# Performance work log

Measured on AMD Instinct MI355X. Metric: run time of the kernel, lower is better.

Reference implementation:

```python
import jax, jax.numpy as jnp
import numpy as np

N_NODES = 100000


def _sage_conv(x, src, dst, W_l, b, W_r):
    """PyG SAGEConv with mean aggregation: lin_l(mean_{j in N(i)} x_j) + lin_r(x_i).
    edge_index[0]=src (message source j), edge_index[1]=dst (target i)."""
    n = x.shape[0]
    # sum of neighbor features per target node, then divide by in-degree
    agg = jax.ops.segment_sum(x[src], dst, num_segments=n)  # [N, F]
    deg = jax.ops.segment_sum(jnp.ones_like(dst, dtype=x.dtype), dst, num_segments=n)
    agg = agg / jnp.maximum(deg, 1.0)[:, None]
    return agg @ W_l + b + x @ W_r


def setup_inputs() -> dict:
    key = jax.random.key(0)
    ks = jax.random.split(key, 8)
    in_c, hid, out = 128, 128, 2
    sc = lambda f: 1.0 / np.sqrt(f)
    x = jax.random.normal(ks[0], (N_NODES, in_c), dtype=jnp.float32)
    edge_index = jax.random.randint(ks[1], (2, 1600000), 0, N_NODES, dtype=jnp.int64)
    return {
        "x": x,
        "edge_index": edge_index,
        "W1_l": jax.random.normal(ks[2], (in_c, hid), dtype=jnp.float32) * sc(in_c),
        "b1": jnp.zeros((hid,), dtype=jnp.float32),
        "W1_r": jax.random.normal(ks[3], (in_c, hid), dtype=jnp.float32) * sc(in_c),
        "W2_l": jax.random.normal(ks[4], (hid, hid), dtype=jnp.float32) * sc(hid),
        "b2": jnp.zeros((hid,), dtype=jnp.float32),
        "W2_r": jax.random.normal(ks[5], (hid, hid), dtype=jnp.float32) * sc(hid),
        "W_fc": jax.random.normal(ks[6], (hid, out), dtype=jnp.float32) * sc(hid),
        "b_fc": jnp.zeros((out,), dtype=jnp.float32),
    }


def reference(x, edge_index, W1_l, b1, W1_r, W2_l, b2, W2_r, W_fc, b_fc):
    src, dst = edge_index[0], edge_index[1]
    # eval mode: dropout is identity
    h = jax.nn.relu(_sage_conv(x, src, dst, W1_l, b1, W1_r))
    h = jax.nn.relu(_sage_conv(h, src, dst, W2_l, b2, W2_r))
    return h @ W_fc + b_fc
```

## Files before the change

### kernel.cpp

```cpp
#include <hip/hip_runtime.h>

#define NF 128
#define SH 9
#define BNODES 512
#define MAXNB 256

typedef unsigned short u16;
typedef unsigned int u32;
using u16x4 = __attribute__((ext_vector_type(4))) u16;
using u16x8 = __attribute__((ext_vector_type(8))) u16;
using s16x8 = __attribute__((ext_vector_type(8))) short;
using f32x4 = __attribute__((ext_vector_type(4))) float;
using u32x4 = __attribute__((ext_vector_type(4))) u32;
using i32x4 = __attribute__((ext_vector_type(4))) int;

__device__ inline float b2f(u16 b) {
    union { u32 u; float f; } c; c.u = (u32)b << 16; return c.f;
}
__device__ inline float lo2f(u32 w) {
    union { u32 u; float f; } c; c.u = w << 16; return c.f;
}
__device__ inline float hi2f(u32 w) {
    union { u32 u; float f; } c; c.u = w & 0xFFFF0000u; return c.f;
}
__device__ inline u16 f2b(float f) {
    union { float f; u32 u; } c; c.f = f;
    u32 u = c.u;
    u += 0x7FFFu + ((u >> 16) & 1u);
    return (u16)(u >> 16);
}
__device__ inline u16x8 nt_load8(const u16* p) {
    u32x4 v = __builtin_nontemporal_load((const u32x4*)p);
    return *(u16x8*)&v;
}
__device__ inline void nt_store8(u16* p, u16x8 v) {
    __builtin_nontemporal_store(*(u32x4*)&v, (u32x4*)p);
}
__device__ inline int padded4(int d) { return (d + 3) & ~3; }

__global__ __launch_bounds__(256) void bhist_kernel(const int* __restrict__ dst,
                                                    int* __restrict__ bcnt, int E, int NB) {
    __shared__ int h[MAXNB];
    int t = threadIdx.x;
    h[t] = 0;
    __syncthreads();
    for (int e = blockIdx.x * 256 + t; e < E; e += gridDim.x * 256)
        atomicAdd(&h[__builtin_nontemporal_load(dst + e) >> SH], 1);
    __syncthreads();
    if (t < NB && h[t]) atomicAdd(&bcnt[t], h[t]);
}

__global__ __launch_bounds__(256) void bscan_kernel(const int* __restrict__ bcnt,
                                                    int* __restrict__ boff,
                                                    int* __restrict__ gcur, int NB, int E) {
    __shared__ int ss[256];
    int t = threadIdx.x;
    int v = (t < NB) ? bcnt[t] : 0;
    ss[t] = v; __syncthreads();
    for (int off = 1; off < 256; off <<= 1) {
        int u = (t >= off) ? ss[t - off] : 0;
        __syncthreads();
        ss[t] += u;
        __syncthreads();
    }
    int excl = ss[t] - v;
    if (t < NB) { boff[t] = excl; gcur[t] = excl; }
    if (t == 0) boff[NB] = E;
}

__global__ __launch_bounds__(256) void scan_excl_kernel(int* __restrict__ a, int nb) {
    __shared__ int ss[256];
    int t = threadIdx.x;
    int v = (t < nb) ? a[t] : 0;
    ss[t] = v; __syncthreads();
    for (int off = 1; off < 256; off <<= 1) {
        int u = (t >= off) ? ss[t - off] : 0;
        __syncthreads();
        ss[t] += u;
        __syncthreads();
    }
    if (t < nb) a[t] = ss[t] - v;
}

__global__ __launch_bounds__(256) void scatter_kernel(
    const int* __restrict__ src, const int* __restrict__ dst,
    int* __restrict__ gcur, u32* __restrict__ pairs, int E, int NB)
{
    __shared__ int hist[MAXNB];
    __shared__ int cstart[256];
    __shared__ int gbase[MAXNB];
    __shared__ u32 stage[4096];
    __shared__ u16 bmap[4096];
    int t = threadIdx.x;
    int base = blockIdx.x * 4096;

    hist[t] = 0;
    __syncthreads();

    u32 packed[16]; int bb[16]; int loff[16];
    #pragma unroll
    for (int j = 0; j < 16; j++) {
        int e = base + j * 256 + t;
        bb[j] = -1;
        if (e < E) {
            int d = __builtin_nontemporal_load(dst + e);
            int s = __builtin_nontemporal_load(src + e);
            int b = d >> SH;
            bb[j] = b;
            packed[j] = ((u32)(d & (BNODES - 1)) << 17) | (u32)s;
            loff[j] = atomicAdd(&hist[b], 1);
        }
    }
    __syncthreads();

    int hv = hist[t];
    cstart[t] = hv; __syncthreads();
    for (int off = 1; off < 256; off <<= 1) {
        int u = (t >= off) ? cstart[t - off] : 0;
        __syncthreads();
        cstart[t] += u;
        __syncthreads();
    }
    int excl = cstart[t] - hv;
    if (t < NB && hv > 0) gbase[t] = atomicAdd(&gcur[t], hv);
    __syncthreads();
    cstart[t] = excl;
    __syncthreads();

    #pragma unroll
    for (int j = 0; j < 16; j++) if (bb[j] >= 0) {
        int pos = cstart[bb[j]] + loff[j];
        stage[pos] = packed[j];
        bmap[pos] = (u16)bb[j];
    }
    __syncthreads();

    int total = min(4096, E - base);
    for (int k = t; k < total; k += 256) {
        u32 p = stage[k];
        int b = bmap[k];
        pairs[gbase[b] + (k - cstart[b])] = p;
    }
}

__global__ __launch_bounds__(256) void degb_kernel(const u32* __restrict__ pairs,
                                                   const int* __restrict__ boff,
                                                   int* __restrict__ deg,
                                                   int* __restrict__ bsumB, int n) {
    __shared__ int dl[BNODES];
    __shared__ int red[256];
    int b = blockIdx.x, t = threadIdx.x;
    for (int i = t; i < BNODES; i += 256) dl[i] = 0;
    __syncthreads();
    int s = boff[b], e = boff[b + 1];
    for (int k = s + t; k < e; k += 256)
        atomicAdd(&dl[__builtin_nontemporal_load(pairs + k) >> 17], 1);
    __syncthreads();
    int nb0 = b << SH;
    int ps = 0;
    for (int i = t; i < BNODES; i += 256) {
        int d = dl[i];
        if (nb0 + i < n) { deg[nb0 + i] = d; ps += padded4(d); }
    }
    red[t] = ps; __syncthreads();
    for (int off = 128; off; off >>= 1) {
        if (t < off) red[t] += red[t + off];
        __syncthreads();
    }
    if (!t) bsumB[b] = red[0];
}

__global__ __launch_bounds__(256) void fillC_kernel(const u32* __restrict__ pairs,
                                                    const int* __restrict__ boff,
                                                    const int* __restrict__ deg,
                                                    const int* __restrict__ bbase,
                                                    int* __restrict__ info,
                                                    int* __restrict__ adj, int n) {
    __shared__ int begl[BNODES];
    __shared__ int curl[BNODES];
    __shared__ int ss[256];
    int b = blockIdx.x, t = threadIdx.x;
    int nb0 = b << SH;
    int i0 = 2 * t, i1 = 2 * t + 1;
    int d0 = 0, d1 = 0;
    if (nb0 + i0 < n) d0 = deg[nb0 + i0];
    if (nb0 + i1 < n) d1 = deg[nb0 + i1];
    int p0 = padded4(d0), p1 = padded4(d1);
    int s = p0 + p1;
    ss[t] = s; __syncthreads();
    for (int off = 1; off < 256; off <<= 1) {
        int u = (t >= off) ? ss[t - off] : 0;
        __syncthreads();
        ss[t] += u;
        __syncthreads();
    }
    int beg0 = bbase[b] + ss[t] - s;
    int beg1 = beg0 + p0;
    if (nb0 + i1 < n) {
        i32x4 w = {beg0, d0, beg1, d1};
        ((i32x4*)info)[(nb0 >> 1) + t] = w;
    } else if (nb0 + i0 < n) {
        info[2 * (nb0 + i0)] = beg0; info[2 * (nb0 + i0) + 1] = d0;
    }
    begl[i0] = beg0; curl[i0] = 0;
    begl[i1] = beg1; curl[i1] = 0;
    if (nb0 + i0 < n) for (int p = d0; p < p0; p++) adj[beg0 + p] = n;
    if (nb0 + i1 < n) for (int p = d1; p < p1; p++) adj[beg1 + p] = n;
    __syncthreads();
    int sE = boff[b], eE = boff[b + 1];
    for (int k = sE + t; k < eE; k += 256) {
        u32 p = __builtin_nontemporal_load(pairs + k);
        int ld = p >> 17, sr = p & 0x1FFFF;
        int pos = atomicAdd(&curl[ld], 1);
        adj[begl[ld] + pos] = sr;
    }
}

__global__ __launch_bounds__(256) void cast_x_kernel(const float* __restrict__ x,
                                                     u16* __restrict__ xb, int n, int nr) {
    int i = blockIdx.x * 256 + threadIdx.x;
    if (i >= nr * (NF / 8)) return;
    int node = i >> 4, ch = i & 15;
    u16x8 o = (u16x8)0;
    if (node < n) {
        const float* p = x + (size_t)node * NF + ch * 8;
        f32x4 v0 = __builtin_nontemporal_load((const f32x4*)p);
        f32x4 v1 = __builtin_nontemporal_load((const f32x4*)(p + 4));
        o[0] = f2b(v0[0]); o[1] = f2b(v0[1]); o[2] = f2b(v0[2]); o[3] = f2b(v0[3]);
        o[4] = f2b(v1[0]); o[5] = f2b(v1[1]); o[6] = f2b(v1[2]); o[7] = f2b(v1[3]);
    }
    *(u16x8*)(xb + (size_t)node * NF + ch * 8) = o;
}

__global__ void cast_wt_kernel(const float* __restrict__ w0, const float* __restrict__ w1,
                               const float* __restrict__ w2, const float* __restrict__ w3,
                               u16* __restrict__ o0, u16* __restrict__ o1,
                               u16* __restrict__ o2, u16* __restrict__ o3) {
    int m = blockIdx.y;
    const float* w = (m == 0) ? w0 : (m == 1) ? w1 : (m == 2) ? w2 : w3;
    u16* o = (m == 0) ? o0 : (m == 1) ? o1 : (m == 2) ? o2 : o3;
    int i = blockIdx.x * 256 + threadIdx.x;
    int k = i >> 7, nc = i & 127;
    o[nc * NF + k] = f2b(w[k * NF + nc]);
}

template <bool FC>
__global__ __launch_bounds__(512) void sage_fused_kernel(
    const u16* __restrict__ xin,
    const int* __restrict__ info,
    const int* __restrict__ adj,
    const u16* __restrict__ Wtl,
    const u16* __restrict__ Wtr,
    const float* __restrict__ bias,
    const float* __restrict__ Wfc,
    const float* __restrict__ bfc,
    u16* __restrict__ hout,
    float* __restrict__ out,
    int n)
{
    constexpr int MT = 128;
    constexpr int LDK = 136;
    __shared__ u16 A_s[MT][LDK];
    __shared__ u16 W_s[NF][LDK];

    int t = threadIdx.x;
    int node0 = blockIdx.x * MT;

    #pragma unroll
    for (int i = 0; i < 4; i++) {
        int idx = t + i * 512;
        int row = idx >> 4, ch = idx & 15;
        *(u16x8*)&W_s[row][ch * 8] = ((const u16x8*)Wtl)[row * 16 + ch];
    }

    {
        int grp = t >> 4, lane = t & 15;
        const char* xbase = (const char*)xin;
        u32 lo16 = (u32)lane * 16;

        for (int j = 0; j < 4; j++) {
            int m = grp * 4 + j;
            int node = node0 + m;
            float L[4] = {0.f, 0.f, 0.f, 0.f}, H[4] = {0.f, 0.f, 0.f, 0.f};
            int dg = 0;
            if (node < n) {
                int2 inf = *(const int2*)(info + 2 * node);
                dg = inf.y;
                const i32x4* ap = (const i32x4*)(adj + inf.x);
                int ng = (dg + 3) >> 2;

#define ROWU(nb) (*(const u32x4*)(xbase + (((u32)(nb) << 8) + lo16)))
#define ACC4(cur) { \
    u32x4 r0 = ROWU(cur[0]), r1 = ROWU(cur[1]), r2 = ROWU(cur[2]), r3 = ROWU(cur[3]); \
    _Pragma("unroll") \
    for (int k = 0; k < 4; k++) { \
        L[k] += (lo2f(r0[k]) + lo2f(r1[k])) + (lo2f(r2[k]) + lo2f(r3[k])); \
        H[k] += (hi2f(r0[k]) + hi2f(r1[k])) + (hi2f(r2[k]) + hi2f(r3[k])); \
    } }
                i32x4 ia, ib;
                if (ng >= 2) {
                    ia = __builtin_nontemporal_load(ap);
                    ib = __builtin_nontemporal_load(ap + 1);
                }
                int g = 0;
                while (g + 2 <= ng) {
                    i32x4 ca = ia, cb = ib;
                    g += 2;
                    if (g + 2 <= ng) {
                        ia = __builtin_nontemporal_load(ap + g);
                        ib = __builtin_nontemporal_load(ap + g + 1);
                    }
                    ACC4(ca);
                    ACC4(cb);
                }
                if (g < ng) {
                    i32x4 ca = __builtin_nontemporal_load(ap + g);
                    ACC4(ca);
                }
#undef ACC4
#undef ROWU
            }
            float invd = 1.0f / fmaxf((float)dg, 1.0f);
            u16x8 o;
            #pragma unroll
            for (int k = 0; k < 4; k++) {
                o[2 * k]     = f2b(L[k] * invd);
                o[2 * k + 1] = f2b(H[k] * invd);
            }
            *(u16x8*)&A_s[m][lane * 8] = o;
        }
    }
    __syncthreads();

    int l = t & 63;
    int lr = l & 15;
    int lko = (l >> 4) * 8;
    int m0 = (t >> 6) * 16;

    f32x4 acc[8];
    #pragma unroll
    for (int f = 0; f < 8; f++) acc[f] = (f32x4)0.f;

    #pragma unroll
    for (int ks = 0; ks < NF; ks += 32) {
        s16x8 a = *(const s16x8*)&A_s[m0 + lr][ks + lko];
        #pragma unroll
        for (int f = 0; f < 8; f++) {
            s16x8 b = *(const s16x8*)&W_s[f * 16 + lr][ks + lko];
            acc[f] = __builtin_amdgcn_mfma_f32_16x16x32_bf16(a, b, acc[f], 0, 0, 0);
        }
    }
    __syncthreads();

    #pragma unroll
    for (int i = 0; i < 4; i++) {
        int idx = t + i * 512;
        int row = idx >> 4, ch = idx & 15;
        *(u16x8*)&W_s[row][ch * 8] = ((const u16x8*)Wtr)[row * 16 + ch];
    }
    #pragma unroll
    for (int i = 0; i < 4; i++) {
        int idx = t + i * 512;
        int row = idx >> 4, ch = idx & 15;
        int node = node0 + row;
        u16x8 v = (u16x8)0;
        if (node < n) v = nt_load8(xin + (size_t)node * NF + ch * 8);
        *(u16x8*)&A_s[row][ch * 8] = v;
    }
    __syncthreads();

    #pragma unroll
    for (int ks = 0; ks < NF; ks += 32) {
        s16x8 a = *(const s16x8*)&A_s[m0 + lr][ks + lko];
        #pragma unroll
        for (int f = 0; f < 8; f++) {
            s16x8 b = *(const s16x8*)&W_s[f * 16 + lr][ks + lko];
            acc[f] = __builtin_amdgcn_mfma_f32_16x16x32_bf16(a, b, acc[f], 0, 0, 0);
        }
    }

    __syncthreads();
    int rowb = m0 + (l >> 4) * 4;
    #pragma unroll
    for (int f = 0; f < 8; f++) {
        float bc = bias[f * 16 + lr];
        #pragma unroll
        for (int r = 0; r < 4; r++) {
            float v = fmaxf(acc[f][r] + bc, 0.f);
            A_s[rowb + r][f * 16 + lr] = f2b(v);
        }
    }
    __syncthreads();

    if (!FC) {
        #pragma unroll
        for (int i = 0; i < 4; i++) {
            int idx = t + i * 512;
            int row = idx >> 4, ch = idx & 15;
            int node = node0 + row;
            if (node < n)
                nt_store8(hout + (size_t)node * NF + ch * 8, *(u16x8*)&A_s[row][ch * 8]);
            else if (node == n)
                nt_store8(hout + (size_t)node * NF + ch * 8, (u16x8)0);
        }
    } else {
        int g = t >> 5, lane = t & 31;
        float2 wfc[4];
        #pragma unroll
        for (int j = 0; j < 4; j++) wfc[j] = ((const float2*)Wfc)[lane * 4 + j];
        float bf0 = bfc[0], bf1 = bfc[1];
        for (int m8 = 0; m8 < 8; m8++) {
            int m = g * 8 + m8;
            float p0 = 0.f, p1 = 0.f;
            #pragma unroll
            for (int j = 0; j < 4; j++) {
                float h = b2f(A_s[m][lane * 4 + j]);
                p0 += h * wfc[j].x;
                p1 += h * wfc[j].y;
            }
            #pragma unroll
            for (int s = 16; s; s >>= 1) {
                p0 += __shfl_down(p0, s, 32);
                p1 += __shfl_down(p1, s, 32);
            }
            int node = node0 + m;
            if (lane == 0 && node < n)
                *(float2*)(out + (size_t)node * 2) = make_float2(p0 + bf0, p1 + bf1);
        }
    }
}

extern "C" void kernel_launch(void* const* d_in, const int* in_sizes, int n_in,
                              void* d_out, int out_size, void* d_ws, size_t ws_size,
                              hipStream_t stream) {
    const float* x   = (const float*)d_in[0];
    const int*   ei  = (const int*)d_in[1];
    const float* W1l = (const float*)d_in[2];
    const float* b1  = (const float*)d_in[3];
    const float* W1r = (const float*)d_in[4];
    const float* W2l = (const float*)d_in[5];
    const float* b2  = (const float*)d_in[6];
    const float* W2r = (const float*)d_in[7];
    const float* Wfc = (const float*)d_in[8];
    const float* bfc = (const float*)d_in[9];

    const int n = in_sizes[0] / NF;
    const int E = in_sizes[1] / 2;
    const int nr = n + 1;
    const int NB = (n + BNODES - 1) >> SH;
    const int* src = ei;
    const int* dst = ei + E;

    u16* xb     = (u16*)d_ws;
    u16* h1     = xb + (size_t)nr * NF;
    u16* Wt1l   = h1 + (size_t)nr * NF;
    u16* Wt1r   = Wt1l + NF * NF;
    u16* Wt2l   = Wt1r + NF * NF;
    u16* Wt2r   = Wt2l + NF * NF;
    int* adj    = (int*)(Wt2r + NF * NF);
    int* deg    = adj + ((size_t)E + 3 * (size_t)n);
    int* info   = deg + n;
    int* bsumB  = info + 2 * (size_t)n;
    int* bcnt   = bsumB + 256;
    int* gcur   = bcnt + 256;
    int* boff   = gcur + 256;
    u32* pairs  = (u32*)(boff + 257);

    (void)hipMemsetAsync(bcnt, 0, 256 * sizeof(int), stream);

    bhist_kernel<<<1024, 256, 0, stream>>>(dst, bcnt, E, NB);
    bscan_kernel<<<1, 256, 0, stream>>>(bcnt, boff, gcur, NB, E);
    scatter_kernel<<<(E + 4095) / 4096, 256, 0, stream>>>(src, dst, gcur, pairs, E, NB);
    degb_kernel<<<NB, 256, 0, stream>>>(pairs, boff, deg, bsumB, n);
    scan_excl_kernel<<<1, 256, 0, stream>>>(bsumB, NB);
    fillC_kernel<<<NB, 256, 0, stream>>>(pairs, boff, deg, bsumB, info, adj, n);

    cast_x_kernel<<<(nr * (NF / 8) + 255) / 256, 256, 0, stream>>>(x, xb, n, nr);
    cast_wt_kernel<<<dim3(64, 4), 256, 0, stream>>>(W1l, W1r, W2l, W2r,
                                                    Wt1l, Wt1r, Wt2l, Wt2r);

    int fb = (nr + 127) / 128;
    sage_fused_kernel<false><<<fb, 512, 0, stream>>>(
        xb, info, adj, Wt1l, Wt1r, b1, nullptr, nullptr, h1, nullptr, n);
    sage_fused_kernel<true><<<fb, 512, 0, stream>>>(
        h1, info, adj, Wt2l, Wt2r, b2, Wfc, bfc, nullptr, (float*)d_out, n);
}
```

Before: 258.2 us.

## Split fused SAGE layer into separate gather kernel and MFMA GEMM kernel

Result: slower. 263.7 us (+2.1%).

```diff
diff --git a/kernel.cpp b/kernel.cpp
--- a/kernel.cpp
+++ b/kernel.cpp
@@ -244,11 +244,72 @@
     o[nc * NF + k] = f2b(w[k * NF + nc]);
 }
 
-template <bool FC>
-__global__ __launch_bounds__(512) void sage_fused_kernel(
-    const u16* __restrict__ xin,
+__global__ __launch_bounds__(256) void gather_kernel(
+    const u16* __restrict__ xb,
     const int* __restrict__ info,
     const int* __restrict__ adj,
+    u16* __restrict__ agg,
+    int n)
+{
+    int node = blockIdx.x * 16 + (threadIdx.x >> 4);
+    if (node >= n) return;
+    int lane = threadIdx.x & 15;
+    const char* xbase = (const char*)xb;
+    u32 lo16 = (u32)lane * 16;
+
+    int2 inf = *(const int2*)(info + 2 * node);
+    int beg = inf.x, deg = inf.y;
+    const i32x4* ap = (const i32x4*)(adj + beg);
+    int ng = (deg + 3) >> 2;
+
+    float L[4] = {0.f, 0.f, 0.f, 0.f}, H[4] = {0.f, 0.f, 0.f, 0.f};
+
+#define ROWU(nb) (*(const u32x4*)(xbase + (((u32)(nb) << 8) + lo16)))
+#define ACC4(cur) { \
+    u32x4 r0 = ROWU(cur[0]), r1 = ROWU(cur[1]), r2 = ROWU(cur[2]), r3 = ROWU(cur[3]); \
+    _Pragma("unroll") \
+    for (int k = 0; k < 4; k++) { \
+        L[k] += (lo2f(r0[k]) + lo2f(r1[k])) + (lo2f(r2[k]) + lo2f(r3[k])); \
+        H[k] += (hi2f(r0[k]) + hi2f(r1[k])) + (hi2f(r2[k]) + hi2f(r3[k])); \
+    } }
+
+    i32x4 ia, ib;
+    if (ng >= 2) {
+        ia = __builtin_nontemporal_load(ap);
+        ib = __builtin_nontemporal_load(ap + 1);
+    }
+    int g = 0;
+    while (g + 2 <= ng) {
+        i32x4 ca = ia, cb = ib;
+        g += 2;
+        if (g + 2 <= ng) {
+            ia = __builtin_nontemporal_load(ap + g);
+            ib = __builtin_nontemporal_load(ap + g + 1);
+        }
+        ACC4(ca);
+        ACC4(cb);
+    }
+    if (g < ng) {
+        i32x4 ca = __builtin_nontemporal_load(ap + g);
+        ACC4(ca);
+    }
+#undef ACC4
+#undef ROWU
+
+    float invd = 1.0f / fmaxf((float)deg, 1.0f);
+    u16x8 o;
+    #pragma unroll
+    for (int k = 0; k < 4; k++) {
+        o[2 * k]     = f2b(L[k] * invd);
+        o[2 * k + 1] = f2b(H[k] * invd);
+    }
+    *(u16x8*)(agg + (size_t)node * NF + lane * 8) = o;
+}
+
+template <bool FC>
+__global__ __launch_bounds__(256) void sage_mfma_kernel(
+    const u16* __restrict__ agg,
+    const u16* __restrict__ selfb,
     const u16* __restrict__ Wtl,
     const u16* __restrict__ Wtr,
     const float* __restrict__ bias,
@@ -258,7 +319,7 @@
     float* __restrict__ out,
     int n)
 {
-    constexpr int MT = 128;
+    constexpr int MT = 64;
     constexpr int LDK = 136;
     __shared__ u16 A_s[MT][LDK];
     __shared__ u16 W_s[NF][LDK];
@@ -267,68 +328,19 @@
     int node0 = blockIdx.x * MT;
 
     #pragma unroll
-    for (int i = 0; i < 4; i++) {
-        int idx = t + i * 512;
+    for (int i = 0; i < 8; i++) {
+        int idx = t + i * 256;
         int row = idx >> 4, ch = idx & 15;
         *(u16x8*)&W_s[row][ch * 8] = ((const u16x8*)Wtl)[row * 16 + ch];
     }
-
-    {
-        int grp = t >> 4, lane = t & 15;
-        const char* xbase = (const char*)xin;
-        u32 lo16 = (u32)lane * 16;
-
-        for (int j = 0; j < 4; j++) {
-            int m = grp * 4 + j;
-            int node = node0 + m;
-            float L[4] = {0.f, 0.f, 0.f, 0.f}, H[4] = {0.f, 0.f, 0.f, 0.f};
-            int dg = 0;
-            if (node < n) {
-                int2 inf = *(const int2*)(info + 2 * node);
-                dg = inf.y;
-                const i32x4* ap = (const i32x4*)(adj + inf.x);
-                int ng = (dg + 3) >> 2;
-
-#define ROWU(nb) (*(const u32x4*)(xbase + (((u32)(nb) << 8) + lo16)))
-#define ACC4(cur) { \
-    u32x4 r0 = ROWU(cur[0]), r1 = ROWU(cur[1]), r2 = ROWU(cur[2]), r3 = ROWU(cur[3]); \
-    _Pragma("unroll") \
-    for (int k = 0; k < 4; k++) { \
-        L[k] += (lo2f(r0[k]) + lo2f(r1[k])) + (lo2f(r2[k]) + lo2f(r3[k])); \
-        H[k] += (hi2f(r0[k]) + hi2f(r1[k])) + (hi2f(r2[k]) + hi2f(r3[k])); \
-    } }
-                i32x4 ia, ib;
-                if (ng >= 2) {
-                    ia = __builtin_nontemporal_load(ap);
-                    ib = __builtin_nontemporal_load(ap + 1);
-                }
-                int g = 0;
-                while (g + 2 <= ng) {
-                    i32x4 ca = ia, cb = ib;
-                    g += 2;
-                    if (g + 2 <= ng) {
-                        ia = __builtin_nontemporal_load(ap + g);
-                        ib = __builtin_nontemporal_load(ap + g + 1);
-                    }
-                    ACC4(ca);
-                    ACC4(cb);
-                }
-                if (g < ng) {
-                    i32x4 ca = __builtin_nontemporal_load(ap + g);
-                    ACC4(ca);
-                }
-#undef ACC4
-#undef ROWU
-            }
-            float invd = 1.0f / fmaxf((float)dg, 1.0f);
-            u16x8 o;
-            #pragma unroll
-            for (int k = 0; k < 4; k++) {
-                o[2 * k]     = f2b(L[k] * invd);
-                o[2 * k + 1] = f2b(H[k] * invd);
-            }
-            *(u16x8*)&A_s[m][lane * 8] = o;
-        }
+    #pragma unroll
+    for (int i = 0; i < 4; i++) {
+        int idx = t + i * 256;
+        int row = idx >> 4, ch = idx & 15;
+        int node = node0 + row;
+        u16x8 v = (u16x8)0;
+        if (node < n) v = nt_load8(agg + (size_t)node * NF + ch * 8);
+        *(u16x8*)&A_s[row][ch * 8] = v;
     }
     __syncthreads();
 
@@ -353,18 +365,18 @@
     __syncthreads();
 
     #pragma unroll
-    for (int i = 0; i < 4; i++) {
-        int idx = t + i * 512;
+    for (int i = 0; i < 8; i++) {
+        int idx = t + i * 256;
         int row = idx >> 4, ch = idx & 15;
         *(u16x8*)&W_s[row][ch * 8] = ((const u16x8*)Wtr)[row * 16 + ch];
     }
     #pragma unroll
     for (int i = 0; i < 4; i++) {
-        int idx = t + i * 512;
+        int idx = t + i * 256;
         int row = idx >> 4, ch = idx & 15;
         int node = node0 + row;
         u16x8 v = (u16x8)0;
-        if (node < n) v = nt_load8(xin + (size_t)node * NF + ch * 8);
+        if (node < n) v = nt_load8(selfb + (size_t)node * NF + ch * 8);
         *(u16x8*)&A_s[row][ch * 8] = v;
     }
     __syncthreads();
@@ -395,7 +407,7 @@
     if (!FC) {
         #pragma unroll
         for (int i = 0; i < 4; i++) {
-            int idx = t + i * 512;
+            int idx = t + i * 256;
             int row = idx >> 4, ch = idx & 15;
             int node = node0 + row;
             if (node < n)
@@ -452,8 +464,9 @@
     const int* dst = ei + E;
 
     u16* xb     = (u16*)d_ws;
-    u16* h1     = xb + (size_t)nr * NF;
-    u16* Wt1l   = h1 + (size_t)nr * NF;
+    u16* agg    = xb  + (size_t)nr * NF;
+    u16* h1     = agg + (size_t)nr * NF;
+    u16* Wt1l   = h1  + (size_t)nr * NF;
     u16* Wt1r   = Wt1l + NF * NF;
     u16* Wt2l   = Wt1r + NF * NF;
     u16* Wt2r   = Wt2l + NF * NF;
@@ -479,9 +492,12 @@
     cast_wt_kernel<<<dim3(64, 4), 256, 0, stream>>>(W1l, W1r, W2l, W2r,
                                                     Wt1l, Wt1r, Wt2l, Wt2r);
 
-    int fb = (nr + 127) / 128;
-    sage_fused_kernel<false><<<fb, 512, 0, stream>>>(
-        xb, info, adj, Wt1l, Wt1r, b1, nullptr, nullptr, h1, nullptr, n);
-    sage_fused_kernel<true><<<fb, 512, 0, stream>>>(
-        h1, info, adj, Wt2l, Wt2r, b2, Wfc, bfc, nullptr, (float*)d_out, n);
-}
+    int gb = (n + 15) / 16;
+    int cb = (nr + 63) / 64;
+    gather_kernel<<<gb, 256, 0, stream>>>(xb, info, adj, agg, n);
+    sage_mfma_kernel<false><<<cb, 256, 0, stream>>>(
+        agg, xb, Wt1l, Wt1r, b1, nullptr, nullptr, h1, nullptr, n);
+    gather_kernel<<<gb, 256, 0, stream>>>(h1, info, adj, agg, n);
+    sage_mfma_kernel<true><<<cb, 256, 0, stream>>>(
+        agg, h1, Wt2l, Wt2r, b2, Wfc, bfc, nullptr, (float*)d_out, n);
+}
```
